# Kernel tuning notes

Hardware: AMD Instinct MI355X
Metric: run time of the kernel (lower is better)

Reference implementation:

```python
import jax, jax.numpy as jnp
import numpy as np

D_MODEL = 256; D_FLOW = 128; D_FFN = 1024
N_HEADS = 8; N_LEVELS = 3; N_POINTS = 4
D_HEAD = D_MODEL // N_HEADS
SHAPES = np.array([[128, 128], [64, 64], [32, 32]], dtype=np.int64)


def setup_inputs():
    key = jax.random.key(0)
    ks = jax.random.split(key, 12)
    N = 2
    LeNin = int((SHAPES[:, 0] * SHAPES[:, 1]).sum())
    Lq = int(SHAPES[0, 0] * SHAPES[0, 1])
    lsi = np.concatenate([[0], np.cumsum(SHAPES[:, 0] * SHAPES[:, 1])[:-1]])
    s = 0.02
    return {
        'src': jax.random.normal(ks[0], (N, LeNin, D_MODEL), jnp.float32),
        'flow': jax.random.normal(ks[1], (N, Lq, D_FLOW), jnp.float32),
        'spatial_shapes': jnp.asarray(SHAPES, jnp.int32),
        'level_start_index': jnp.asarray(lsi, jnp.int32),
        'w_value': jax.random.normal(ks[2], (D_MODEL, D_MODEL), jnp.float32) * s,
        'b_value': jnp.zeros((D_MODEL,), jnp.float32),
        'w_off': jax.random.normal(ks[3], (D_FLOW, N_HEADS * N_LEVELS * N_POINTS * 2), jnp.float32) * s,
        'b_off': jax.random.normal(ks[4], (N_HEADS * N_LEVELS * N_POINTS * 2,), jnp.float32) * 0.5,
        'w_attn': jax.random.normal(ks[5], (D_FLOW, N_HEADS * N_LEVELS * N_POINTS), jnp.float32) * s,
        'b_attn': jnp.zeros((N_HEADS * N_LEVELS * N_POINTS,), jnp.float32),
        'w_out': jax.random.normal(ks[6], (D_MODEL, D_MODEL), jnp.float32) * s,
        'b_out': jnp.zeros((D_MODEL,), jnp.float32),
        'gamma': jnp.ones((D_MODEL,), jnp.float32),
        'beta': jnp.zeros((D_MODEL,), jnp.float32),
        'w1': jax.random.normal(ks[7], (D_MODEL, D_FFN), jnp.float32) * s,
        'b1': jnp.zeros((D_FFN,), jnp.float32),
        'w2': jax.random.normal(ks[8], (D_FFN, D_MODEL), jnp.float32) * s,
        'b2': jnp.zeros((D_MODEL,), jnp.float32),
    }


def _bilinear_level(v, xy, H, W):
    # v: [N, nh, H*W, dh]; xy: [N, Lq, nh, np, 2] normalized to [0,1]
    # grid_sample(align_corners=False) semantics: pixel = loc * size - 0.5, zero padding
    N, Lq = xy.shape[0], xy.shape[1]
    x = xy[..., 0] * W - 0.5
    y = xy[..., 1] * H - 0.5
    x0 = jnp.floor(x); y0 = jnp.floor(y)
    dx = x - x0; dy = y - y0
    acc = jnp.zeros((N, N_HEADS, Lq * N_POINTS, v.shape[-1]), v.dtype)
    corners = ((x0, y0, (1 - dx) * (1 - dy)),
               (x0 + 1, y0, dx * (1 - dy)),
               (x0, y0 + 1, (1 - dx) * dy),
               (x0 + 1, y0 + 1, dx * dy))
    for ix, iy, w in corners:
        valid = (ix >= 0) & (ix <= W - 1) & (iy >= 0) & (iy <= H - 1)
        xi = jnp.clip(ix, 0, W - 1).astype(jnp.int32)
        yi = jnp.clip(iy, 0, H - 1).astype(jnp.int32)
        idx = (yi * W + xi).transpose(0, 2, 1, 3).reshape(N, N_HEADS, Lq * N_POINTS)
        g = jnp.take_along_axis(v, idx[..., None], axis=2)  # [N, nh, Lq*np, dh]
        wv = (w * valid).transpose(0, 2, 1, 3).reshape(N, N_HEADS, Lq * N_POINTS, 1)
        acc = acc + wv * g
    return acc


def reference(src, flow, spatial_shapes, level_start_index, w_value, b_value,
              w_off, b_off, w_attn, b_attn, w_out, b_out, gamma, beta, w1, b1, w2, b2):
    ss = np.asarray(jax.device_get(spatial_shapes))
    lsi = np.asarray(jax.device_get(level_start_index))
    N, LeNin, _ = src.shape
    Lq = flow.shape[1]
    value = (src @ w_value + b_value).reshape(N, LeNin, N_HEADS, D_HEAD)
    off = (flow @ w_off + b_off).reshape(N, Lq, N_HEADS, N_LEVELS, N_POINTS, 2)
    attn = jax.nn.softmax((flow @ w_attn + b_attn).reshape(N, Lq, N_HEADS, N_LEVELS * N_POINTS), axis=-1)
    attn = attn.reshape(N, Lq, N_HEADS, N_LEVELS, N_POINTS)
    # reference points on level-0 grid (valid_ratios == 1)
    H0, W0 = int(ss[0, 0]), int(ss[0, 1])
    ry, rx = jnp.meshgrid(jnp.linspace(0.5, H0 - 0.5, H0) / H0,
                          jnp.linspace(0.5, W0 - 0.5, W0) / W0, indexing='ij')
    ref = jnp.stack([rx.reshape(-1), ry.reshape(-1)], -1)  # [Lq, 2] (x, y)
    norm = jnp.asarray(np.stack([ss[:, 1], ss[:, 0]], -1), jnp.float32)  # [nl, 2] = (W, H)
    loc = ref[None, :, None, None, None, :] + off / norm[None, None, None, :, None, :]
    acc = jnp.zeros((N, Lq, N_HEADS, D_HEAD), src.dtype)
    for l in range(N_LEVELS):
        H, W = int(ss[l, 0]), int(ss[l, 1])
        st = int(lsi[l])
        v = value[:, st:st + H * W].transpose(0, 2, 1, 3)  # [N, nh, HW, dh]
        s_l = _bilinear_level(v, loc[:, :, :, l], H, W).reshape(N, N_HEADS, Lq, N_POINTS, D_HEAD)
        acc = acc + jnp.einsum('bhqpd,bqhp->bqhd', s_l, attn[:, :, :, l])
    src2 = acc.reshape(N, Lq, D_MODEL) @ w_out + b_out
    x = src2  # dropout is identity at inference
    mu = x.mean(-1, keepdims=True)
    var = ((x - mu) ** 2).mean(-1, keepdims=True)
    ln = (x - mu) / jnp.sqrt(var + 1e-5) * gamma + beta
    ffn = jax.nn.relu(ln @ w1 + b1) @ w2 + b2
    return x + ffn
```

## Files before the change

### kernel.cpp

```cpp
#include <hip/hip_runtime.h>
#include <cstdint>
#include <cstddef>

#define D_MODEL  256
#define D_FLOW   128
#define D_FFN    1024
#define N_HEADS  8
#define N_LEVELS 3
#define N_POINTS 4
#define D_HEAD   32
#define LQ       16384
#define LENIN    21504
#define NB       2

typedef unsigned short ushort;
typedef __attribute__((ext_vector_type(8))) short bf16x8;
typedef __attribute__((ext_vector_type(4))) float f32x4;

__device__ __forceinline__ ushort f2b(float f) {
    uint32_t u = __float_as_uint(f);
    uint32_t r = (u + 0x7fffu + ((u >> 16) & 1u)) >> 16;
    return (ushort)r;
}

__device__ __forceinline__ void gl_lds16(const void* g, void* l) {
    __builtin_amdgcn_global_load_lds(
        (const __attribute__((address_space(1))) unsigned int*)g,
        (__attribute__((address_space(3))) unsigned int*)l,
        16, 0, 0);
}

template<bool A_FP32, bool RELU, bool RESID, bool OUT_BF16>
__global__ __launch_bounds__(256)
void mfma_gemm(const void* __restrict__ Ain, const ushort* __restrict__ Bt,
               const float* __restrict__ bias, const float* __restrict__ resid,
               void* __restrict__ Cout, int N, int K)
{
    __shared__ ushort As[128 * 64];
    __shared__ ushort Bs[128 * 64];

    const int tid  = threadIdx.x;
    const int wave = tid >> 6;
    const int lane = tid & 63;
    const int quad = lane >> 4;
    const int l16  = lane & 15;
    const int wr   = (wave >> 1) * 64;
    const int wc   = (wave & 1) * 64;

    const int nx = gridDim.x;
    int lin = blockIdx.y * nx + blockIdx.x;
    const int total = nx * gridDim.y;
    if ((total & 7) == 0) lin = (lin & 7) * (total >> 3) + (lin >> 3);
    const int by = lin / nx;
    const int bx = lin - by * nx;
    const int bm = by * 128;
    const int bn = bx * 128;

    const int sr  = lane >> 3;
    const int sc  = lane & 7;
    const int gch = sc ^ sr;

    f32x4 acc[4][4] = {};
    const int swz = l16 & 7;

    for (int k0 = 0; k0 < K; k0 += 64) {
        __syncthreads();
        if (A_FP32) {
            const float* Af = (const float*)Ain;
#pragma unroll
            for (int i = 0; i < 4; ++i) {
                const int row = wave * 32 + i * 8 + sr;
                const float* p = Af + (size_t)(bm + row) * K + k0 + gch * 8;
                const float4 v0 = *(const float4*)(p);
                const float4 v1 = *(const float4*)(p + 4);
                bf16x8 pk;
                pk[0] = (short)f2b(v0.x); pk[1] = (short)f2b(v0.y);
                pk[2] = (short)f2b(v0.z); pk[3] = (short)f2b(v0.w);
                pk[4] = (short)f2b(v1.x); pk[5] = (short)f2b(v1.y);
                pk[6] = (short)f2b(v1.z); pk[7] = (short)f2b(v1.w);
                *(bf16x8*)&As[(size_t)row * 64 + sc * 8] = pk;
            }
        } else {
            const ushort* Ab = (const ushort*)Ain;
#pragma unroll
            for (int i = 0; i < 4; ++i) {
                const int row = wave * 32 + i * 8;
                gl_lds16(Ab + (size_t)(bm + row + sr) * K + k0 + gch * 8,
                         As + (size_t)row * 64);
            }
        }
#pragma unroll
        for (int i = 0; i < 4; ++i) {
            const int row = wave * 32 + i * 8;
            gl_lds16(Bt + (size_t)(bn + row + sr) * K + k0 + gch * 8,
                     Bs + (size_t)row * 64);
        }
        __syncthreads();

#pragma unroll
        for (int kk = 0; kk < 2; ++kk) {
            bf16x8 af[4], bfr[4];
#pragma unroll
            for (int mi = 0; mi < 4; ++mi) {
                const int p = (kk * 4 + quad) ^ swz;
                af[mi] = *(const bf16x8*)&As[(wr + mi * 16 + l16) * 64 + p * 8];
            }
#pragma unroll
            for (int ni = 0; ni < 4; ++ni) {
                const int p = (kk * 4 + quad) ^ swz;
                bfr[ni] = *(const bf16x8*)&Bs[(wc + ni * 16 + l16) * 64 + p * 8];
            }
#pragma unroll
            for (int mi = 0; mi < 4; ++mi)
#pragma unroll
                for (int ni = 0; ni < 4; ++ni)
                    acc[mi][ni] = __builtin_amdgcn_mfma_f32_16x16x32_bf16(
                        af[mi], bfr[ni], acc[mi][ni], 0, 0, 0);
        }
    }

#pragma unroll
    for (int mi = 0; mi < 4; ++mi) {
#pragma unroll
        for (int ni = 0; ni < 4; ++ni) {
            const int col = bn + wc + ni * 16 + l16;
            const float bb = bias[col];
#pragma unroll
            for (int r = 0; r < 4; ++r) {
                const int row = bm + wr + mi * 16 + quad * 4 + r;
                const size_t idx = (size_t)row * N + col;
                float c = acc[mi][ni][r] + bb;
                if (RELU)  c = fmaxf(c, 0.f);
                if (RESID) c += resid[idx];
                if (OUT_BF16) ((ushort*)Cout)[idx] = f2b(c);
                else          ((float*)Cout)[idx]  = c;
            }
        }
    }
}

__global__ __launch_bounds__(256)
void gemm_ln_k(const ushort* __restrict__ A, const ushort* __restrict__ Bt,
               const float* __restrict__ bias, const float* __restrict__ gamma,
               const float* __restrict__ beta,
               float* __restrict__ xout, ushort* __restrict__ lnout, int K)
{
    __shared__ ushort As[64 * 32];
    __shared__ ushort Bs[256 * 32];
    __shared__ float  sS[64][33];
    __shared__ float  sS2[64][33];
    __shared__ float  sMu[64], sRi[64];

    const int tid  = threadIdx.x;
    const int wave = tid >> 6;
    const int lane = tid & 63;
    const int quad = lane >> 4;
    const int l16  = lane & 15;
    const int wr   = (wave >> 1) * 32;
    const int wc   = (wave & 1) * 128;
    const int bm   = blockIdx.x * 64;

    const int sr  = lane >> 2;
    const int sc  = lane & 3;
    const int gch = sc ^ (sr & 3);

    f32x4 acc[2][8] = {};
    const int swz = l16 & 3;

    for (int k0 = 0; k0 < K; k0 += 32) {
        __syncthreads();
        gl_lds16(A + (size_t)(bm + wave * 16 + sr) * K + k0 + gch * 8,
                 As + wave * 16 * 32);
#pragma unroll
        for (int i = 0; i < 4; ++i) {
            const int row = wave * 64 + i * 16;
            gl_lds16(Bt + (size_t)(row + sr) * K + k0 + gch * 8,
                     Bs + (size_t)row * 32);
        }
        __syncthreads();

        bf16x8 af[2], bfr[8];
#pragma unroll
        for (int mi = 0; mi < 2; ++mi)
            af[mi] = *(const bf16x8*)&As[(wr + mi * 16 + l16) * 32 + ((quad ^ swz) << 3)];
#pragma unroll
        for (int ni = 0; ni < 8; ++ni)
            bfr[ni] = *(const bf16x8*)&Bs[(wc + ni * 16 + l16) * 32 + ((quad ^ swz) << 3)];
#pragma unroll
        for (int mi = 0; mi < 2; ++mi)
#pragma unroll
            for (int ni = 0; ni < 8; ++ni)
                acc[mi][ni] = __builtin_amdgcn_mfma_f32_16x16x32_bf16(
                    af[mi], bfr[ni], acc[mi][ni], 0, 0, 0);
    }

    float bias8[8], g8[8], b8[8];
#pragma unroll
    for (int ni = 0; ni < 8; ++ni) {
        const int col = wc + ni * 16 + l16;
        bias8[ni] = bias[col];
        g8[ni]    = gamma[col];
        b8[ni]    = beta[col];
    }

#pragma unroll
    for (int mi = 0; mi < 2; ++mi)
#pragma unroll
        for (int r = 0; r < 4; ++r) {
            float s = 0.f, s2 = 0.f;
#pragma unroll
            for (int ni = 0; ni < 8; ++ni) {
                const float c = acc[mi][ni][r] + bias8[ni];
                s += c; s2 += c * c;
            }
            const int row = wr + mi * 16 + quad * 4 + r;
            sS[row][(wave & 1) * 16 + l16]  = s;
            sS2[row][(wave & 1) * 16 + l16] = s2;
        }
    __syncthreads();

    if (tid < 64) {
        float s = 0.f, s2 = 0.f;
#pragma unroll
        for (int j = 0; j < 32; ++j) { s += sS[tid][j]; s2 += sS2[tid][j]; }
        const float mu  = s * (1.f / 256.f);
        const float var = s2 * (1.f / 256.f) - mu * mu;
        sMu[tid] = mu;
        sRi[tid] = rsqrtf(var + 1e-5f);
    }
    __syncthreads();

#pragma unroll
    for (int mi = 0; mi < 2; ++mi)
#pragma unroll
        for (int r = 0; r < 4; ++r) {
            const int lrow = wr + mi * 16 + quad * 4 + r;
            const int grow = bm + lrow;
            const float mu = sMu[lrow], ri = sRi[lrow];
#pragma unroll
            for (int ni = 0; ni < 8; ++ni) {
                const int col = wc + ni * 16 + l16;
                const float c = acc[mi][ni][r] + bias8[ni];
                xout[(size_t)grow * 256 + col]  = c;
                lnout[(size_t)grow * 256 + col] = f2b((c - mu) * ri * g8[ni] + b8[ni]);
            }
        }
}

__global__ __launch_bounds__(512, 2)
void ffn_fused_k(const ushort* __restrict__ ln, const ushort* __restrict__ w1T,
                 const ushort* __restrict__ w2R, const float* __restrict__ b1v,
                 const float* __restrict__ b2v, float* __restrict__ out)
{
    extern __shared__ ushort smem[];
    ushort* const w1s0 = smem;
    ushort* const w1s1 = smem + 16384;
    ushort* const hs0  = smem + 32768;
    ushort* const hs1  = smem + 40960;

    const int tid  = threadIdx.x;
    const int wave = tid >> 6;
    const int lane = tid & 63;
    const int quad = lane >> 4;
    const int l16  = lane & 15;
    const int bm   = blockIdx.x * 128;

    const int R0g1 = (wave >> 1) * 32;
    const int C0g1 = (wave & 1) * 32;
    const int M0   = (wave & 1) * 64;
    const int N0   = (wave >> 1) * 64;

    bf16x8 afA[2][8];
#pragma unroll
    for (int mt = 0; mt < 2; ++mt)
#pragma unroll
        for (int kk = 0; kk < 8; ++kk) {
            const int row = bm + R0g1 + mt * 16 + l16;
            afA[mt][kk] = *(const bf16x8*)&ln[(size_t)row * 256 + (kk * 4 + quad) * 8];
        }
#pragma unroll
    for (int i = 0; i < 4; ++i) {
        const int r0 = (wave * 4 + i) * 2;
        const int r  = r0 + (lane >> 5);
        gl_lds16(w1T + (size_t)r * 256 + (((lane & 31) ^ (r & 7)) << 3),
                 w1s0 + r0 * 256);
    }
    __syncthreads();

    f32x4 acc2[4][4] = {};

#pragma unroll 1
    for (int c = 0; c < 16; ++c) {
        ushort* const w1cur = (c & 1) ? w1s1 : w1s0;
        ushort* const w1nxt = (c & 1) ? w1s0 : w1s1;
        ushort* const hcur  = (c & 1) ? hs1  : hs0;
        ushort* const hprv  = (c & 1) ? hs0  : hs1;

        if (c < 15) {
#pragma unroll
            for (int i = 0; i < 4; ++i) {
                const int r0 = (wave * 4 + i) * 2;
                const int r  = r0 + (lane >> 5);
                gl_lds16(w1T + (size_t)((c + 1) * 64 + r) * 256
                             + (((lane & 31) ^ (r & 7)) << 3),
                         w1nxt + r0 * 256);
            }
        }

        bf16x8 w2f[2][4];
        if (c >= 1) {
#pragma unroll
            for (int kk = 0; kk < 2; ++kk) {
                const int g = kk * 4 + quad;
                const ushort* base = w2R + ((size_t)((c - 1) * 8 + g)) * 2048;
#pragma unroll
                for (int nt = 0; nt < 4; ++nt) {
                    const int n = N0 + nt * 16 + l16;
                    w2f[kk][nt] = *(const bf16x8*)(base + n * 8);
                }
            }
        }

        f32x4 acc1[2][2] = {};
#pragma unroll
        for (int kk = 0; kk < 8; ++kk) {
            bf16x8 wf[2];
#pragma unroll
            for (int nt = 0; nt < 2; ++nt) {
                const int n = C0g1 + nt * 16 + l16;
                wf[nt] = *(const bf16x8*)
                    &w1cur[n * 256 + (((kk * 4 + quad) ^ (n & 7)) << 3)];
            }
#pragma unroll
            for (int mt = 0; mt < 2; ++mt)
#pragma unroll
                for (int nt = 0; nt < 2; ++nt)
                    acc1[mt][nt] = __builtin_amdgcn_mfma_f32_16x16x32_bf16(
                        wf[nt], afA[mt][kk], acc1[mt][nt], 0, 0, 0);
        }

        {
            float4 bb[2];
#pragma unroll
            for (int nt = 0; nt < 2; ++nt)
                bb[nt] = *(const float4*)&b1v[c * 64 + C0g1 + nt * 16 + quad * 4];
#pragma unroll
            for (int mt = 0; mt < 2; ++mt) {
                const int m = R0g1 + mt * 16 + l16;
#pragma unroll
                for (int nt = 0; nt < 2; ++nt) {
                    const int oct = (C0g1 >> 2) + nt * 4 + quad;
                    ushort4 pk;
                    pk.x = f2b(fmaxf(acc1[mt][nt][0] + bb[nt].x, 0.f));
                    pk.y = f2b(fmaxf(acc1[mt][nt][1] + bb[nt].y, 0.f));
                    pk.z = f2b(fmaxf(acc1[mt][nt][2] + bb[nt].z, 0.f));
                    pk.w = f2b(fmaxf(acc1[mt][nt][3] + bb[nt].w, 0.f));
                    *(ushort4*)&hcur[m * 64 + ((oct ^ ((m & 7) << 1)) << 2)] = pk;
                }
            }
        }

        if (c >= 1) {
#pragma unroll
            for (int kk = 0; kk < 2; ++kk) {
                const int g = kk * 4 + quad;
                bf16x8 hf[4];
#pragma unroll
                for (int mt = 0; mt < 4; ++mt) {
                    const int m = M0 + mt * 16 + l16;
                    hf[mt] = *(const bf16x8*)&hprv[m * 64 + ((g ^ (m & 7)) << 3)];
                }
#pragma unroll
                for (int mt = 0; mt < 4; ++mt)
#pragma unroll
                    for (int nt = 0; nt < 4; ++nt)
                        acc2[mt][nt] = __builtin_amdgcn_mfma_f32_16x16x32_bf16(
                            w2f[kk][nt], hf[mt], acc2[mt][nt], 0, 0, 0);
            }
        }
        __syncthreads();
    }

    {
        bf16x8 w2f[2][4];
#pragma unroll
        for (int kk = 0; kk < 2; ++kk) {
            const int g = kk * 4 + quad;
            const ushort* base = w2R + ((size_t)(15 * 8 + g)) * 2048;
#pragma unroll
            for (int nt = 0; nt < 4; ++nt) {
                const int n = N0 + nt * 16 + l16;
                w2f[kk][nt] = *(const bf16x8*)(base + n * 8);
            }
        }
#pragma unroll
        for (int kk = 0; kk < 2; ++kk) {
            const int g = kk * 4 + quad;
            bf16x8 hf[4];
#pragma unroll
            for (int mt = 0; mt < 4; ++mt) {
                const int m = M0 + mt * 16 + l16;
                hf[mt] = *(const bf16x8*)&hs1[m * 64 + ((g ^ (m & 7)) << 3)];
            }
#pragma unroll
            for (int mt = 0; mt < 4; ++mt)
#pragma unroll
                for (int nt = 0; nt < 4; ++nt)
                    acc2[mt][nt] = __builtin_amdgcn_mfma_f32_16x16x32_bf16(
                        w2f[kk][nt], hf[mt], acc2[mt][nt], 0, 0, 0);
        }
    }

#pragma unroll
    for (int mt = 0; mt < 4; ++mt) {
        const int row = bm + M0 + mt * 16 + l16;
#pragma unroll
        for (int nt = 0; nt < 4; ++nt) {
            const int col = N0 + nt * 16 + quad * 4;
            float4* p = (float4*)(out + (size_t)row * 256 + col);
            const float4 b4 = *(const float4*)&b2v[col];
            float4 v = *p;
            v.x = v.x + acc2[mt][nt][0] + b4.x;
            v.y = v.y + acc2[mt][nt][1] + b4.y;
            v.z = v.z + acc2[mt][nt][2] + b4.z;
            v.w = v.w + acc2[mt][nt][3] + b4.w;
            *p = v;
        }
    }
}

__device__ __forceinline__ void acc8(float* a, uint4 g, float w) {
    a[0] = fmaf(w, __uint_as_float(g.x << 16), a[0]);
    a[1] = fmaf(w, __uint_as_float(g.x), a[1]);
    a[2] = fmaf(w, __uint_as_float(g.y << 16), a[2]);
    a[3] = fmaf(w, __uint_as_float(g.y), a[3]);
    a[4] = fmaf(w, __uint_as_float(g.z << 16), a[4]);
    a[5] = fmaf(w, __uint_as_float(g.z), a[5]);
    a[6] = fmaf(w, __uint_as_float(g.w << 16), a[6]);
    a[7] = fmaf(w, __uint_as_float(g.w), a[7]);
}

__global__ __launch_bounds__(256)
void sample_k(const ushort* __restrict__ value, const ushort* __restrict__ projc,
              ushort* __restrict__ acc)
{
    __shared__ float sOff[8][192];
    __shared__ float sAttn[8][96];

    const int tid = threadIdx.x;
    const int bid = blockIdx.x;
    const int bq0 = (((bid & 7) << 9) | (bid >> 3)) << 3;

    for (int i = tid; i < 8 * 288; i += 256) {
        const int qw = i / 288, j = i - qw * 288;
        const float v = __uint_as_float((uint32_t)projc[(size_t)(bq0 + qw) * 384 + j] << 16);
        if (j < 192) sOff[qw][j] = v;
        else         sAttn[qw][j - 192] = v;
    }
    __syncthreads();

    if (tid < 64) {
        const int qw = tid >> 3, h = tid & 7;
        float* row = &sAttn[qw][h * 12];
        float m = row[0];
#pragma unroll
        for (int j = 1; j < 12; ++j) m = fmaxf(m, row[j]);
        float s = 0.f;
#pragma unroll
        for (int j = 0; j < 12; ++j) { const float e = __expf(row[j] - m); row[j] = e; s += e; }
        const float inv = 1.f / s;
#pragma unroll
        for (int j = 0; j < 12; ++j) row[j] *= inv;
    }
    __syncthreads();

    const int wave = tid >> 6, lane = tid & 63;
    const int qh = lane >> 5;
    const int h  = (lane >> 2) & 7;
    const int cg = lane & 3;
    const int qw = wave * 2 + qh;
    const int bq = bq0 + qw;
    const int n  = bq >> 14;
    const int q  = bq & 16383;

    const float qx = (float)(q & 127) + 0.5f;
    const float qy = (float)(q >> 7) + 0.5f;

    const int LSIc[3] = {0, 16384, 20480};

    float a[8] = {0.f, 0.f, 0.f, 0.f, 0.f, 0.f, 0.f, 0.f};
    const ushort* vbase = value + (size_t)n * LENIN * D_MODEL + h * D_HEAD + cg * 8;

#pragma unroll
    for (int l = 0; l < N_LEVELS; ++l) {
        const int   W     = 128 >> l;
        const int   SH    = 7 - l;
        const float scale = 1.f / (float)(1 << l);
        const float cx    = qx * scale - 0.5f;
        const float cy    = qy * scale - 0.5f;
        const ushort* vlev = vbase + ((size_t)LSIc[l] << 8);
#pragma unroll
        for (int p = 0; p < N_POINTS; ++p) {
            const int ob = (h * N_LEVELS + l) * (N_POINTS * 2) + p * 2;
            const float aw = sAttn[qw][h * 12 + l * 4 + p];
            const float x = cx + sOff[qw][ob];
            const float y = cy + sOff[qw][ob + 1];
            const float x0f = floorf(x), y0f = floorf(y);
            const int x0 = (int)x0f, y0 = (int)y0f;
            const float dx = x - x0f, dy = y - y0f;
            float wx1 = dx * aw, wx0 = aw - wx1;
            float wy1 = dy,      wy0 = 1.f - dy;
            if ((unsigned)x0       > (unsigned)(W - 1)) wx0 = 0.f;
            if ((unsigned)(x0 + 1) > (unsigned)(W - 1)) wx1 = 0.f;
            if ((unsigned)y0       > (unsigned)(W - 1)) wy0 = 0.f;
            if ((unsigned)(y0 + 1) > (unsigned)(W - 1)) wy1 = 0.f;
            const int xi0 = min(max(x0, 0), W - 1);
            const int xi1 = min(max(x0 + 1, 0), W - 1);
            const int yi0 = min(max(y0, 0), W - 1);
            const int yi1 = min(max(y0 + 1, 0), W - 1);
            const uint4 g00 = *(const uint4*)(vlev + ((size_t)((yi0 << SH) + xi0) << 8));
            const uint4 g01 = *(const uint4*)(vlev + ((size_t)((yi0 << SH) + xi1) << 8));
            const uint4 g10 = *(const uint4*)(vlev + ((size_t)((yi1 << SH) + xi0) << 8));
            const uint4 g11 = *(const uint4*)(vlev + ((size_t)((yi1 << SH) + xi1) << 8));
            acc8(a, g00, wx0 * wy0);
            acc8(a, g01, wx1 * wy0);
            acc8(a, g10, wx0 * wy1);
            acc8(a, g11, wx1 * wy1);
        }
    }

    const uint32_t o0 = (uint32_t)f2b(a[0]) | ((uint32_t)f2b(a[1]) << 16);
    const uint32_t o1 = (uint32_t)f2b(a[2]) | ((uint32_t)f2b(a[3]) << 16);
    const uint32_t o2 = (uint32_t)f2b(a[4]) | ((uint32_t)f2b(a[5]) << 16);
    const uint32_t o3 = (uint32_t)f2b(a[6]) | ((uint32_t)f2b(a[7]) << 16);
    const uint4 ov = {o0, o1, o2, o3};
    *(uint4*)(acc + (size_t)bq * D_MODEL + h * D_HEAD + cg * 8) = ov;
}

__global__ __launch_bounds__(256)
void prep_all_k(const float* __restrict__ w_value, const float* __restrict__ w_out,
                const float* __restrict__ w1, const float* __restrict__ w2,
                const float* __restrict__ w_off, const float* __restrict__ b_off,
                const float* __restrict__ w_attn, const float* __restrict__ b_attn,
                ushort* __restrict__ wvT, ushort* __restrict__ woT,
                ushort* __restrict__ w1T, ushort* __restrict__ w2R,
                ushort* __restrict__ wcT, float* __restrict__ biasc)
{
    int i = blockIdx.x * 256 + threadIdx.x;
    if (i < 65536) {
        const int k = i >> 8, n = i & 255;
        wvT[(size_t)n * 256 + k] = f2b(w_value[i]);
        return;
    }
    i -= 65536;
    if (i < 65536) {
        const int k = i >> 8, n = i & 255;
        woT[(size_t)n * 256 + k] = f2b(w_out[i]);
        return;
    }
    i -= 65536;
    if (i < 262144) {
        const int k = i >> 10, n = i & 1023;
        w1T[(size_t)n * 256 + k] = f2b(w1[i]);
        return;
    }
    i -= 262144;
    if (i < 262144) {
        const int k = i >> 8, n = i & 255;
        w2R[(size_t)(k >> 3) * 2048 + n * 8 + (k & 7)] = f2b(w2[i]);
        return;
    }
    i -= 262144;
    if (i < 49152) {
        const int nn = i >> 7, k = i & 127;
        float v = 0.f;
        if (nn < 192)      v = w_off[(size_t)k * 192 + nn];
        else if (nn < 288) v = w_attn[(size_t)k * 96 + (nn - 192)];
        wcT[i] = f2b(v);
        return;
    }
    i -= 49152;
    if (i < 384) {
        float b = 0.f;
        if (i < 192)      b = b_off[i];
        else if (i < 288) b = b_attn[i - 192];
        biasc[i] = b;
    }
}

extern "C" void kernel_launch(void* const* d_in, const int* in_sizes, int n_in,
                              void* d_out, int out_size, void* d_ws, size_t ws_size,
                              hipStream_t stream)
{
    const float* src     = (const float*)d_in[0];
    const float* flow    = (const float*)d_in[1];
    const float* w_value = (const float*)d_in[4];
    const float* b_value = (const float*)d_in[5];
    const float* w_off   = (const float*)d_in[6];
    const float* b_off   = (const float*)d_in[7];
    const float* w_attn  = (const float*)d_in[8];
    const float* b_attn  = (const float*)d_in[9];
    const float* w_out   = (const float*)d_in[10];
    const float* b_out   = (const float*)d_in[11];
    const float* gamma   = (const float*)d_in[12];
    const float* beta    = (const float*)d_in[13];
    const float* w1      = (const float*)d_in[14];
    const float* b1      = (const float*)d_in[15];
    const float* w2      = (const float*)d_in[16];
    const float* b2      = (const float*)d_in[17];
    float* out = (float*)d_out;
    char*  wsb = (char*)d_ws;

    ushort* value_bf = (ushort*)(wsb);
    ushort* acc_bf   = (ushort*)(wsb + 22020096);
    ushort* projc_bf = (ushort*)(wsb + 67108864);
    ushort* ln_bf    = (ushort*)(wsb + 67108864);
    ushort* wvT      = (ushort*)(wsb + 92274688);
    ushort* woT      = (ushort*)(wsb + 92405760);
    ushort* w1T      = (ushort*)(wsb + 92536832);
    ushort* w2R      = (ushort*)(wsb + 93061120);
    ushort* wcT      = (ushort*)(wsb + 93585408);
    float*  biasc    = (float*) (wsb + 93683712);

    const int Mq = NB * LQ;
    const int Mv = NB * LENIN;

    static bool ffn_attr_done = false;
    if (!ffn_attr_done) {
        hipFuncSetAttribute((const void*)ffn_fused_k,
                            hipFuncAttributeMaxDynamicSharedMemorySize, 98304);
        ffn_attr_done = true;
    }

    prep_all_k<<<2754, 256, 0, stream>>>(w_value, w_out, w1, w2,
                                         w_off, b_off, w_attn, b_attn,
                                         wvT, woT, w1T, w2R, wcT, biasc);

    mfma_gemm<true, false, false, true><<<dim3(2, Mv / 128), 256, 0, stream>>>(
        src, wvT, b_value, nullptr, value_bf, 256, 256);

    mfma_gemm<true, false, false, true><<<dim3(3, Mq / 128), 256, 0, stream>>>(
        flow, wcT, biasc, nullptr, projc_bf, 384, 128);

    sample_k<<<Mq / 8, 256, 0, stream>>>(value_bf, projc_bf, acc_bf);

    gemm_ln_k<<<Mq / 64, 256, 0, stream>>>(
        acc_bf, woT, b_out, gamma, beta, out, ln_bf, 256);

    ffn_fused_k<<<Mq / 128, 512, 98304, stream>>>(ln_bf, w1T, w2R, b1, b2, out);
}
```

Measured before the change: 269.8 us.

## Fuse output projection and LayerNorm into the fused FFN kernel

Removes the separate gemm_ln kernel and computes the output-projection GEMM, bias and LayerNorm inside ffn_fused_k. The normalised rows are staged in swizzled LDS and read back as A fragments. The pre-LN residual stays in the acc2 registers, and the second FFN GEMM accumulates onto it. This avoids writing and re-reading the fp32 residual and the bf16 LN activations through global memory, and saves one kernel launch. In exchange the FFN kernel does more work per block before its pipelined loop starts, and it needs slightly more dynamic LDS.

```diff
diff --git a/kernel.cpp b/kernel.cpp
--- a/kernel.cpp
+++ b/kernel.cpp
@@ -139,120 +139,21 @@
     }
 }
 
-__global__ __launch_bounds__(256)
-void gemm_ln_k(const ushort* __restrict__ A, const ushort* __restrict__ Bt,
-               const float* __restrict__ bias, const float* __restrict__ gamma,
-               const float* __restrict__ beta,
-               float* __restrict__ xout, ushort* __restrict__ lnout, int K)
-{
-    __shared__ ushort As[64 * 32];
-    __shared__ ushort Bs[256 * 32];
-    __shared__ float  sS[64][33];
-    __shared__ float  sS2[64][33];
-    __shared__ float  sMu[64], sRi[64];
-
-    const int tid  = threadIdx.x;
-    const int wave = tid >> 6;
-    const int lane = tid & 63;
-    const int quad = lane >> 4;
-    const int l16  = lane & 15;
-    const int wr   = (wave >> 1) * 32;
-    const int wc   = (wave & 1) * 128;
-    const int bm   = blockIdx.x * 64;
-
-    const int sr  = lane >> 2;
-    const int sc  = lane & 3;
-    const int gch = sc ^ (sr & 3);
-
-    f32x4 acc[2][8] = {};
-    const int swz = l16 & 3;
-
-    for (int k0 = 0; k0 < K; k0 += 32) {
-        __syncthreads();
-        gl_lds16(A + (size_t)(bm + wave * 16 + sr) * K + k0 + gch * 8,
-                 As + wave * 16 * 32);
-#pragma unroll
-        for (int i = 0; i < 4; ++i) {
-            const int row = wave * 64 + i * 16;
-            gl_lds16(Bt + (size_t)(row + sr) * K + k0 + gch * 8,
-                     Bs + (size_t)row * 32);
-        }
-        __syncthreads();
-
-        bf16x8 af[2], bfr[8];
-#pragma unroll
-        for (int mi = 0; mi < 2; ++mi)
-            af[mi] = *(const bf16x8*)&As[(wr + mi * 16 + l16) * 32 + ((quad ^ swz) << 3)];
-#pragma unroll
-        for (int ni = 0; ni < 8; ++ni)
-            bfr[ni] = *(const bf16x8*)&Bs[(wc + ni * 16 + l16) * 32 + ((quad ^ swz) << 3)];
-#pragma unroll
-        for (int mi = 0; mi < 2; ++mi)
-#pragma unroll
-            for (int ni = 0; ni < 8; ++ni)
-                acc[mi][ni] = __builtin_amdgcn_mfma_f32_16x16x32_bf16(
-                    af[mi], bfr[ni], acc[mi][ni], 0, 0, 0);
-    }
-
-    float bias8[8], g8[8], b8[8];
-#pragma unroll
-    for (int ni = 0; ni < 8; ++ni) {
-        const int col = wc + ni * 16 + l16;
-        bias8[ni] = bias[col];
-        g8[ni]    = gamma[col];
-        b8[ni]    = beta[col];
-    }
-
-#pragma unroll
-    for (int mi = 0; mi < 2; ++mi)
-#pragma unroll
-        for (int r = 0; r < 4; ++r) {
-            float s = 0.f, s2 = 0.f;
-#pragma unroll
-            for (int ni = 0; ni < 8; ++ni) {
-                const float c = acc[mi][ni][r] + bias8[ni];
-                s += c; s2 += c * c;
-            }
-            const int row = wr + mi * 16 + quad * 4 + r;
-            sS[row][(wave & 1) * 16 + l16]  = s;
-            sS2[row][(wave & 1) * 16 + l16] = s2;
-        }
-    __syncthreads();
-
-    if (tid < 64) {
-        float s = 0.f, s2 = 0.f;
-#pragma unroll
-        for (int j = 0; j < 32; ++j) { s += sS[tid][j]; s2 += sS2[tid][j]; }
-        const float mu  = s * (1.f / 256.f);
-        const float var = s2 * (1.f / 256.f) - mu * mu;
-        sMu[tid] = mu;
-        sRi[tid] = rsqrtf(var + 1e-5f);
-    }
-    __syncthreads();
-
-#pragma unroll
-    for (int mi = 0; mi < 2; ++mi)
-#pragma unroll
-        for (int r = 0; r < 4; ++r) {
-            const int lrow = wr + mi * 16 + quad * 4 + r;
-            const int grow = bm + lrow;
-            const float mu = sMu[lrow], ri = sRi[lrow];
-#pragma unroll
-            for (int ni = 0; ni < 8; ++ni) {
-                const int col = wc + ni * 16 + l16;
-                const float c = acc[mi][ni][r] + bias8[ni];
-                xout[(size_t)grow * 256 + col]  = c;
-                lnout[(size_t)grow * 256 + col] = f2b((c - mu) * ri * g8[ni] + b8[ni]);
-            }
-        }
-}
-
 __global__ __launch_bounds__(512, 2)
-void ffn_fused_k(const ushort* __restrict__ ln, const ushort* __restrict__ w1T,
-                 const ushort* __restrict__ w2R, const float* __restrict__ b1v,
-                 const float* __restrict__ b2v, float* __restrict__ out)
+void ffn_fused_k(const ushort* __restrict__ accb, const ushort* __restrict__ woT,
+                 const ushort* __restrict__ w1T,  const ushort* __restrict__ w2R,
+                 const float* __restrict__ b_out, const float* __restrict__ gamma,
+                 const float* __restrict__ beta,  const float* __restrict__ b1v,
+                 const float* __restrict__ b2v,   float* __restrict__ out)
 {
     extern __shared__ ushort smem[];
+    ushort* const aS  = smem;
+    ushort* const wS  = smem + 8192;
+    float*  const sP  = (float*)smem;
+    float*  const sQ  = (float*)(smem + 4352);
+    ushort* const lnS = smem + 16384;
+    float*  const sMu = (float*)(smem + 49152);
+    float*  const sRi = (float*)(smem + 49408);
     ushort* const w1s0 = smem;
     ushort* const w1s1 = smem + 16384;
     ushort* const hs0  = smem + 32768;
@@ -265,19 +166,103 @@
     const int l16  = lane & 15;
     const int bm   = blockIdx.x * 128;
 
+    const int M0   = (wave & 1) * 64;
+    const int N0   = (wave >> 1) * 64;
     const int R0g1 = (wave >> 1) * 32;
     const int C0g1 = (wave & 1) * 32;
-    const int M0   = (wave & 1) * 64;
-    const int N0   = (wave >> 1) * 64;
-
-    bf16x8 afA[2][8];
-#pragma unroll
-    for (int mt = 0; mt < 2; ++mt)
-#pragma unroll
-        for (int kk = 0; kk < 8; ++kk) {
-            const int row = bm + R0g1 + mt * 16 + l16;
-            afA[mt][kk] = *(const bf16x8*)&ln[(size_t)row * 256 + (kk * 4 + quad) * 8];
-        }
+
+    const int sr  = lane >> 3;
+    const int sc  = lane & 7;
+    const int gch = sc ^ sr;
+
+    f32x4 acc2[4][4] = {};
+
+    for (int k0 = 0; k0 < 256; k0 += 64) {
+        __syncthreads();
+#pragma unroll
+        for (int i = 0; i < 2; ++i) {
+            const int r0 = wave * 16 + i * 8;
+            gl_lds16(accb + (size_t)(bm + r0 + sr) * 256 + k0 + gch * 8,
+                     aS + r0 * 64);
+        }
+#pragma unroll
+        for (int i = 0; i < 4; ++i) {
+            const int r0 = wave * 32 + i * 8;
+            gl_lds16(woT + (size_t)(r0 + sr) * 256 + k0 + gch * 8,
+                     wS + r0 * 64);
+        }
+        __syncthreads();
+
+#pragma unroll
+        for (int kk = 0; kk < 2; ++kk) {
+            const int g = kk * 4 + quad;
+            bf16x8 af[4], wf[4];
+#pragma unroll
+            for (int mt = 0; mt < 4; ++mt) {
+                const int m = M0 + mt * 16 + l16;
+                af[mt] = *(const bf16x8*)&aS[m * 64 + ((g ^ (m & 7)) << 3)];
+            }
+#pragma unroll
+            for (int nt = 0; nt < 4; ++nt) {
+                const int n = N0 + nt * 16 + l16;
+                wf[nt] = *(const bf16x8*)&wS[n * 64 + ((g ^ (n & 7)) << 3)];
+            }
+#pragma unroll
+            for (int mt = 0; mt < 4; ++mt)
+#pragma unroll
+                for (int nt = 0; nt < 4; ++nt)
+                    acc2[mt][nt] = __builtin_amdgcn_mfma_f32_16x16x32_bf16(
+                        wf[nt], af[mt], acc2[mt][nt], 0, 0, 0);
+        }
+    }
+    __syncthreads();
+
+    {
+        float4 bo[4];
+#pragma unroll
+        for (int nt = 0; nt < 4; ++nt)
+            bo[nt] = *(const float4*)&b_out[N0 + nt * 16 + quad * 4];
+        const int widx = (wave >> 1) * 4 + quad;
+#pragma unroll
+        for (int mt = 0; mt < 4; ++mt) {
+            const int m = M0 + mt * 16 + l16;
+            float s = 0.f, s2 = 0.f;
+#pragma unroll
+            for (int nt = 0; nt < 4; ++nt) {
+                acc2[mt][nt][0] += bo[nt].x;
+                acc2[mt][nt][1] += bo[nt].y;
+                acc2[mt][nt][2] += bo[nt].z;
+                acc2[mt][nt][3] += bo[nt].w;
+#pragma unroll
+                for (int r = 0; r < 4; ++r) {
+                    const float c = acc2[mt][nt][r];
+                    s += c; s2 += c * c;
+                }
+            }
+            sP[m * 17 + widx] = s;
+            sQ[m * 17 + widx] = s2;
+        }
+    }
+    __syncthreads();
+
+    if (tid < 128) {
+        float s = 0.f, s2 = 0.f;
+#pragma unroll
+        for (int j = 0; j < 16; ++j) { s += sP[tid * 17 + j]; s2 += sQ[tid * 17 + j]; }
+        const float mu  = s * (1.f / 256.f);
+        const float var = s2 * (1.f / 256.f) - mu * mu;
+        sMu[tid] = mu;
+        sRi[tid] = rsqrtf(var + 1e-5f);
+    }
+    __syncthreads();
+
+    float mu4[4], ri4[4];
+#pragma unroll
+    for (int mt = 0; mt < 4; ++mt) {
+        const int m = M0 + mt * 16 + l16;
+        mu4[mt] = sMu[m]; ri4[mt] = sRi[m];
+    }
+
 #pragma unroll
     for (int i = 0; i < 4; ++i) {
         const int r0 = (wave * 4 + i) * 2;
@@ -285,9 +270,37 @@
         gl_lds16(w1T + (size_t)r * 256 + (((lane & 31) ^ (r & 7)) << 3),
                  w1s0 + r0 * 256);
     }
+
+#pragma unroll
+    for (int mt = 0; mt < 4; ++mt) {
+        const int m = M0 + mt * 16 + l16;
+        const float mu = mu4[mt], ri = ri4[mt];
+#pragma unroll
+        for (int nt = 0; nt < 4; ++nt) {
+            const int col0 = N0 + nt * 16 + quad * 4;
+            const float4 g4 = *(const float4*)&gamma[col0];
+            const float4 b4 = *(const float4*)&beta[col0];
+            ushort4 pk;
+            pk.x = f2b((acc2[mt][nt][0] - mu) * ri * g4.x + b4.x);
+            pk.y = f2b((acc2[mt][nt][1] - mu) * ri * g4.y + b4.y);
+            pk.z = f2b((acc2[mt][nt][2] - mu) * ri * g4.z + b4.z);
+            pk.w = f2b((acc2[mt][nt][3] - mu) * ri * g4.w + b4.w);
+            const int c8 = col0 >> 3;
+            *(ushort4*)&lnS[m * 256 + ((c8 ^ (m & 7)) << 3) + (quad & 1) * 4] = pk;
+        }
+    }
     __syncthreads();
 
-    f32x4 acc2[4][4] = {};
+    bf16x8 afA[2][8];
+#pragma unroll
+    for (int mt = 0; mt < 2; ++mt)
+#pragma unroll
+        for (int kk = 0; kk < 8; ++kk) {
+            const int row = R0g1 + mt * 16 + l16;
+            afA[mt][kk] = *(const bf16x8*)
+                &lnS[row * 256 + (((kk * 4 + quad) ^ (row & 7)) << 3)];
+        }
+    __syncthreads();
 
 #pragma unroll 1
     for (int c = 0; c < 16; ++c) {
@@ -417,14 +430,13 @@
 #pragma unroll
         for (int nt = 0; nt < 4; ++nt) {
             const int col = N0 + nt * 16 + quad * 4;
-            float4* p = (float4*)(out + (size_t)row * 256 + col);
             const float4 b4 = *(const float4*)&b2v[col];
-            float4 v = *p;
-            v.x = v.x + acc2[mt][nt][0] + b4.x;
-            v.y = v.y + acc2[mt][nt][1] + b4.y;
-            v.z = v.z + acc2[mt][nt][2] + b4.z;
-            v.w = v.w + acc2[mt][nt][3] + b4.w;
-            *p = v;
+            float4 v;
+            v.x = acc2[mt][nt][0] + b4.x;
+            v.y = acc2[mt][nt][1] + b4.y;
+            v.z = acc2[mt][nt][2] + b4.z;
+            v.w = acc2[mt][nt][3] + b4.w;
+            *(float4*)(out + (size_t)row * 256 + col) = v;
         }
     }
 }
@@ -614,7 +626,6 @@
     ushort* value_bf = (ushort*)(wsb);
     ushort* acc_bf   = (ushort*)(wsb + 22020096);
     ushort* projc_bf = (ushort*)(wsb + 67108864);
-    ushort* ln_bf    = (ushort*)(wsb + 67108864);
     ushort* wvT      = (ushort*)(wsb + 92274688);
     ushort* woT      = (ushort*)(wsb + 92405760);
     ushort* w1T      = (ushort*)(wsb + 92536832);
@@ -628,7 +639,7 @@
     static bool ffn_attr_done = false;
     if (!ffn_attr_done) {
         hipFuncSetAttribute((const void*)ffn_fused_k,
-                            hipFuncAttributeMaxDynamicSharedMemorySize, 98304);
+                            hipFuncAttributeMaxDynamicSharedMemorySize, 99328);
         ffn_attr_done = true;
     }
 
@@ -644,8 +655,6 @@
 
     sample_k<<<Mq / 8, 256, 0, stream>>>(value_bf, projc_bf, acc_bf);
 
-    gemm_ln_k<<<Mq / 64, 256, 0, stream>>>(
-        acc_bf, woT, b_out, gamma, beta, out, ln_bf, 256);
-
-    ffn_fused_k<<<Mq / 128, 512, 98304, stream>>>(ln_bf, w1T, w2R, b1, b2, out);
-}
+    ffn_fused_k<<<Mq / 128, 512, 99328, stream>>>(
+        acc_bf, woT, w1T, w2R, b_out, gamma, beta, b1, b2, out);
+}
```

New measurement: 250.4 us. -7.2%, faster.
